# Kernel optimization log

Measured on AMD Instinct MI355X. Metric: run time of the kernel, lower is better.

The kernel has to match this reference:

```python
import jax, jax.numpy as jnp
import numpy as np

B, T, D, K = 8, 2048, 128, 2


def setup_inputs() -> dict:
    key = jax.random.key(0)
    k1, k2 = jax.random.split(key)
    z = jax.random.normal(k1, (B, T, D), dtype=jnp.float32)
    gt_dT = jax.random.normal(k2, (B, T, T, K), dtype=jnp.float32)
    sigma = jnp.ones((K,), dtype=jnp.float32)
    return {"z": z, "gt_dT": gt_dT, "sigma": sigma}


def reference(z, gt_dT, sigma):
    # z: [B,T,D], gt_dT: [B,T,T,K], sigma: [K]
    two_sigma_sq = 2.0 * sigma * sigma                    # [K]
    kernel = jnp.sum(gt_dT * gt_dT / two_sigma_sq, axis=-1)  # [B,T,T]
    w = jnp.exp(-kernel)                                  # [B,T,T]
    z2 = jnp.einsum('btd,btd->bt', z, z)                  # [B,T] squared norms
    w_row_col_sum = jnp.sum(w, axis=2) + jnp.sum(w, axis=1)  # [B,T]
    term1_plus_3 = jnp.einsum('bt,bt->b', z2, w_row_col_sum)  # [B]
    wz = jnp.einsum('bij,bjd->bid', w, z)                 # [B,T,D]
    term2 = jnp.einsum('bid,bid->b', wz, z)               # [B]
    Tn = z.shape[1]
    loss = jnp.mean(term1_plus_3 - 2.0 * term2) / (Tn * Tn)
    return loss
```

## Files before the change

kernel.cpp:

```cpp
#include <hip/hip_runtime.h>


#define T_DIM 2048
#define D_DIM 128
#define B_DIM 8
#define NTHREADS 256
#define GSTRIDE 36

typedef short s16x8 __attribute__((ext_vector_type(8)));
typedef float f32x4 __attribute__((ext_vector_type(4)));

__device__ __forceinline__ unsigned short f2bf(float x) {
    unsigned int u = __float_as_uint(x);
    u += 0x7fffu + ((u >> 16) & 1u);
    return (unsigned short)(u >> 16);
}

__global__ __launch_bounds__(NTHREADS)
void patch_prep(const float* __restrict__ z, unsigned short* __restrict__ zbf,
                float* __restrict__ z2, float* __restrict__ out) {
    if (blockIdx.x == 0 && threadIdx.x == 0) out[0] = 0.0f;
    const int row = blockIdx.x * 8 + (threadIdx.x >> 5);
    const int c4  = threadIdx.x & 31;
    float4 v = ((const float4*)(z + (size_t)row * D_DIM))[c4];
    ushort4 p;
    p.x = f2bf(v.x); p.y = f2bf(v.y); p.z = f2bf(v.z); p.w = f2bf(v.w);
    ((ushort4*)(zbf + (size_t)row * D_DIM))[c4] = p;
    float s = v.x*v.x + v.y*v.y + v.z*v.z + v.w*v.w;
    #pragma unroll
    for (int m = 16; m >= 1; m >>= 1) s += __shfl_xor(s, m);
    if (c4 == 0) z2[row] = s;
}

__global__ __launch_bounds__(NTHREADS)
void patch_loss_main(const unsigned short* __restrict__ zbf,
                     const float* __restrict__ z2,
                     const float* __restrict__ gt,
                     const float* __restrict__ sigma,
                     float* __restrict__ out) {
    __shared__ float gram[4][32][GSTRIDE];
    __shared__ float red[4];

    const int tid  = threadIdx.x;
    const int wave = tid >> 6;
    const int lane = tid & 63;
    const int c = lane & 15;
    const int q = lane >> 4;

    const int b  = blockIdx.z;
    const int i0 = blockIdx.y * 64 + (wave >> 1) * 32;
    const int j0 = blockIdx.x * 64 + (wave & 1) * 32;

    f32x4 g[8];
    const float* gbase = gt + ((size_t)b * T_DIM + i0 + q * 4) * (2 * T_DIM)
                            + (size_t)(j0 + 2 * c) * 2;
    #pragma unroll
    for (int fi = 0; fi < 2; ++fi)
        #pragma unroll
        for (int rr = 0; rr < 4; ++rr)
            g[fi * 4 + rr] = __builtin_nontemporal_load(
                (const f32x4*)(gbase + ((size_t)fi * 16 + rr) * (2 * T_DIM)));

    const unsigned short* zi = zbf + ((size_t)b * T_DIM + i0) * D_DIM;
    const unsigned short* zj = zbf + ((size_t)b * T_DIM + j0) * D_DIM;
    f32x4 acc[2][2] = {};
    #pragma unroll
    for (int kk = 0; kk < 4; ++kk) {
        const int co = kk * 32 + q * 8;
        s16x8 fa0 = *(const s16x8*)(zi + (size_t)(c)      * D_DIM + co);
        s16x8 fa1 = *(const s16x8*)(zi + (size_t)(16 + c) * D_DIM + co);
        s16x8 fb0 = *(const s16x8*)(zj + (size_t)(c)      * D_DIM + co);
        s16x8 fb1 = *(const s16x8*)(zj + (size_t)(16 + c) * D_DIM + co);
        acc[0][0] = __builtin_amdgcn_mfma_f32_16x16x32_bf16(fa0, fb0, acc[0][0], 0, 0, 0);
        acc[0][1] = __builtin_amdgcn_mfma_f32_16x16x32_bf16(fa0, fb1, acc[0][1], 0, 0, 0);
        acc[1][0] = __builtin_amdgcn_mfma_f32_16x16x32_bf16(fa1, fb0, acc[1][0], 0, 0, 0);
        acc[1][1] = __builtin_amdgcn_mfma_f32_16x16x32_bf16(fa1, fb1, acc[1][1], 0, 0, 0);
    }

    #pragma unroll
    for (int fi = 0; fi < 2; ++fi)
        #pragma unroll
        for (int r = 0; r < 4; ++r) {
            gram[wave][fi * 16 + q * 4 + r][c]      = acc[fi][0][r];
            gram[wave][fi * 16 + q * 4 + r][16 + c] = acc[fi][1][r];
        }
    __syncthreads();

    const float s0 = sigma[0], s1 = sigma[1];
    const float a0 = 0.5f / (s0 * s0);
    const float a1 = 0.5f / (s1 * s1);
    const float z2j0 = z2[(size_t)b * T_DIM + j0 + 2 * c];
    const float z2j1 = z2[(size_t)b * T_DIM + j0 + 2 * c + 1];

    float facc = 0.0f;
    #pragma unroll
    for (int fi = 0; fi < 2; ++fi)
        #pragma unroll
        for (int rr = 0; rr < 4; ++rr) {
            const int il = fi * 16 + q * 4 + rr;
            const float zzi = z2[(size_t)b * T_DIM + i0 + il];
            float2 s = *(const float2*)&gram[wave][il][2 * c];
            f32x4 gv = g[fi * 4 + rr];
            const float t0 = gv[0] * gv[0] * a0 + gv[1] * gv[1] * a1;
            const float t1 = gv[2] * gv[2] * a0 + gv[3] * gv[3] * a1;
            facc += __expf(-t0) * (zzi + z2j0 - 2.0f * s.x)
                  + __expf(-t1) * (zzi + z2j1 - 2.0f * s.y);
        }

    #pragma unroll
    for (int m = 32; m >= 1; m >>= 1) facc += __shfl_xor(facc, m);
    if (lane == 0) red[wave] = facc;
    __syncthreads();
    if (tid == 0) {
        const float scale = 1.0f / ((float)B_DIM * (float)T_DIM * (float)T_DIM);
        atomicAdd(out, (red[0] + red[1] + red[2] + red[3]) * scale);
    }
}

extern "C" void kernel_launch(void* const* d_in, const int* in_sizes, int n_in,
                              void* d_out, int out_size, void* d_ws, size_t ws_size,
                              hipStream_t stream) {
    const float* z     = (const float*)d_in[0];
    const float* gt    = (const float*)d_in[1];
    const float* sigma = (const float*)d_in[2];
    float* out = (float*)d_out;

    unsigned short* zbf = (unsigned short*)d_ws;
    float* z2 = (float*)((char*)d_ws + (size_t)B_DIM * T_DIM * D_DIM * 2);

    patch_prep<<<(B_DIM * T_DIM) / 8, NTHREADS, 0, stream>>>(z, zbf, z2, out);
    dim3 grid(T_DIM / 64, T_DIM / 64, B_DIM);
    patch_loss_main<<<grid, NTHREADS, 0, stream>>>(zbf, z2, gt, sigma, out);
}
```

Before: 414.6 us.

## Enlarge block tile to 128x128 and loop each wave over four column tiles

Each wave now owns 32 rows and walks four 32-column tiles inside the block. Its row-side bf16 fragments and z2 row norms are loaded once and kept in registers across those tiles. This cuts redundant z loads, block launches and atomic adds, since the grid shrinks by a factor of four. In exchange there is more register pressure and fewer blocks for latency hiding, and the LDS gram exchange between lanes now runs without a barrier.

```diff
diff --git a/kernel.cpp b/kernel.cpp
--- a/kernel.cpp
+++ b/kernel.cpp
@@ -47,65 +47,86 @@
     const int c = lane & 15;
     const int q = lane >> 4;
 
-    const int b  = blockIdx.z;
-    const int i0 = blockIdx.y * 64 + (wave >> 1) * 32;
-    const int j0 = blockIdx.x * 64 + (wave & 1) * 32;
+    const int b     = blockIdx.z;
+    const int i0    = blockIdx.y * 128 + wave * 32;
+    const int jbase = blockIdx.x * 128;
 
-    f32x4 g[8];
-    const float* gbase = gt + ((size_t)b * T_DIM + i0 + q * 4) * (2 * T_DIM)
-                            + (size_t)(j0 + 2 * c) * 2;
+    const float s0 = sigma[0], s1 = sigma[1];
+    const float a0 = 0.5f / (s0 * s0);
+    const float a1 = 0.5f / (s1 * s1);
+
+    const unsigned short* zi = zbf + ((size_t)b * T_DIM + i0) * D_DIM;
+    s16x8 fa[2][4];
+    #pragma unroll
+    for (int kk = 0; kk < 4; ++kk) {
+        const int co = kk * 32 + q * 8;
+        fa[0][kk] = *(const s16x8*)(zi + (size_t)(c)      * D_DIM + co);
+        fa[1][kk] = *(const s16x8*)(zi + (size_t)(16 + c) * D_DIM + co);
+    }
+    float z2i[2][4];
     #pragma unroll
     for (int fi = 0; fi < 2; ++fi)
         #pragma unroll
         for (int rr = 0; rr < 4; ++rr)
-            g[fi * 4 + rr] = __builtin_nontemporal_load(
-                (const f32x4*)(gbase + ((size_t)fi * 16 + rr) * (2 * T_DIM)));
-
-    const unsigned short* zi = zbf + ((size_t)b * T_DIM + i0) * D_DIM;
-    const unsigned short* zj = zbf + ((size_t)b * T_DIM + j0) * D_DIM;
-    f32x4 acc[2][2] = {};
-    #pragma unroll
-    for (int kk = 0; kk < 4; ++kk) {
-        const int co = kk * 32 + q * 8;
-        s16x8 fa0 = *(const s16x8*)(zi + (size_t)(c)      * D_DIM + co);
-        s16x8 fa1 = *(const s16x8*)(zi + (size_t)(16 + c) * D_DIM + co);
-        s16x8 fb0 = *(const s16x8*)(zj + (size_t)(c)      * D_DIM + co);
-        s16x8 fb1 = *(const s16x8*)(zj + (size_t)(16 + c) * D_DIM + co);
-        acc[0][0] = __builtin_amdgcn_mfma_f32_16x16x32_bf16(fa0, fb0, acc[0][0], 0, 0, 0);
-        acc[0][1] = __builtin_amdgcn_mfma_f32_16x16x32_bf16(fa0, fb1, acc[0][1], 0, 0, 0);
-        acc[1][0] = __builtin_amdgcn_mfma_f32_16x16x32_bf16(fa1, fb0, acc[1][0], 0, 0, 0);
-        acc[1][1] = __builtin_amdgcn_mfma_f32_16x16x32_bf16(fa1, fb1, acc[1][1], 0, 0, 0);
-    }
-
-    #pragma unroll
-    for (int fi = 0; fi < 2; ++fi)
-        #pragma unroll
-        for (int r = 0; r < 4; ++r) {
-            gram[wave][fi * 16 + q * 4 + r][c]      = acc[fi][0][r];
-            gram[wave][fi * 16 + q * 4 + r][16 + c] = acc[fi][1][r];
-        }
-    __syncthreads();
-
-    const float s0 = sigma[0], s1 = sigma[1];
-    const float a0 = 0.5f / (s0 * s0);
-    const float a1 = 0.5f / (s1 * s1);
-    const float z2j0 = z2[(size_t)b * T_DIM + j0 + 2 * c];
-    const float z2j1 = z2[(size_t)b * T_DIM + j0 + 2 * c + 1];
+            z2i[fi][rr] = z2[(size_t)b * T_DIM + i0 + fi * 16 + q * 4 + rr];
 
     float facc = 0.0f;
     #pragma unroll
-    for (int fi = 0; fi < 2; ++fi)
+    for (int jj = 0; jj < 4; ++jj) {
+        const int j0 = jbase + jj * 32;
+
+        const unsigned short* zj = zbf + ((size_t)b * T_DIM + j0) * D_DIM;
+        s16x8 fb0[4], fb1[4];
         #pragma unroll
-        for (int rr = 0; rr < 4; ++rr) {
-            const int il = fi * 16 + q * 4 + rr;
-            const float zzi = z2[(size_t)b * T_DIM + i0 + il];
-            float2 s = *(const float2*)&gram[wave][il][2 * c];
-            f32x4 gv = g[fi * 4 + rr];
-            const float t0 = gv[0] * gv[0] * a0 + gv[1] * gv[1] * a1;
-            const float t1 = gv[2] * gv[2] * a0 + gv[3] * gv[3] * a1;
-            facc += __expf(-t0) * (zzi + z2j0 - 2.0f * s.x)
-                  + __expf(-t1) * (zzi + z2j1 - 2.0f * s.y);
+        for (int kk = 0; kk < 4; ++kk) {
+            const int co = kk * 32 + q * 8;
+            fb0[kk] = *(const s16x8*)(zj + (size_t)(c)      * D_DIM + co);
+            fb1[kk] = *(const s16x8*)(zj + (size_t)(16 + c) * D_DIM + co);
         }
+
+        f32x4 g[8];
+        const float* gbase = gt + ((size_t)b * T_DIM + i0 + q * 4) * (2 * T_DIM)
+                                + (size_t)(j0 + 2 * c) * 2;
+        #pragma unroll
+        for (int fi = 0; fi < 2; ++fi)
+            #pragma unroll
+            for (int rr = 0; rr < 4; ++rr)
+                g[fi * 4 + rr] = __builtin_nontemporal_load(
+                    (const f32x4*)(gbase + ((size_t)fi * 16 + rr) * (2 * T_DIM)));
+
+        f32x4 acc[2][2] = {};
+        #pragma unroll
+        for (int kk = 0; kk < 4; ++kk) {
+            acc[0][0] = __builtin_amdgcn_mfma_f32_16x16x32_bf16(fa[0][kk], fb0[kk], acc[0][0], 0, 0, 0);
+            acc[0][1] = __builtin_amdgcn_mfma_f32_16x16x32_bf16(fa[0][kk], fb1[kk], acc[0][1], 0, 0, 0);
+            acc[1][0] = __builtin_amdgcn_mfma_f32_16x16x32_bf16(fa[1][kk], fb0[kk], acc[1][0], 0, 0, 0);
+            acc[1][1] = __builtin_amdgcn_mfma_f32_16x16x32_bf16(fa[1][kk], fb1[kk], acc[1][1], 0, 0, 0);
+        }
+
+        #pragma unroll
+        for (int fi = 0; fi < 2; ++fi)
+            #pragma unroll
+            for (int r = 0; r < 4; ++r) {
+                gram[wave][fi * 16 + q * 4 + r][c]      = acc[fi][0][r];
+                gram[wave][fi * 16 + q * 4 + r][16 + c] = acc[fi][1][r];
+            }
+
+        const float z2j0 = z2[(size_t)b * T_DIM + j0 + 2 * c];
+        const float z2j1 = z2[(size_t)b * T_DIM + j0 + 2 * c + 1];
+
+        #pragma unroll
+        for (int fi = 0; fi < 2; ++fi)
+            #pragma unroll
+            for (int rr = 0; rr < 4; ++rr) {
+                const int il = fi * 16 + q * 4 + rr;
+                float2 s = *(const float2*)&gram[wave][il][2 * c];
+                f32x4 gv = g[fi * 4 + rr];
+                const float t0 = gv[0] * gv[0] * a0 + gv[1] * gv[1] * a1;
+                const float t1 = gv[2] * gv[2] * a0 + gv[3] * gv[3] * a1;
+                facc += __expf(-t0) * (z2i[fi][rr] + z2j0 - 2.0f * s.x)
+                      + __expf(-t1) * (z2i[fi][rr] + z2j1 - 2.0f * s.y);
+            }
+    }
 
     #pragma unroll
     for (int m = 32; m >= 1; m >>= 1) facc += __shfl_xor(facc, m);
@@ -129,6 +150,6 @@
     float* z2 = (float*)((char*)d_ws + (size_t)B_DIM * T_DIM * D_DIM * 2);
 
     patch_prep<<<(B_DIM * T_DIM) / 8, NTHREADS, 0, stream>>>(z, zbf, z2, out);
-    dim3 grid(T_DIM / 64, T_DIM / 64, B_DIM);
+    dim3 grid(T_DIM / 128, T_DIM / 128, B_DIM);
     patch_loss_main<<<grid, NTHREADS, 0, stream>>>(zbf, z2, gt, sigma, out);
 }
```

New measurement: 360.4 us. -13.1%, faster.
